# Kernel optimization log

Measured on AMD Instinct MI355X. Metric: run time of the kernel, lower is better.

Reference implementation:

```python
import jax, jax.numpy as jnp
import numpy as np

B, D, C, P = 1024, 768, 150, 64  # batch, in_feats, num_labels, proj2 dim
POS_M, NEG_M = 0.7, 1.4


def setup_inputs() -> dict:
    key = jax.random.key(0)
    ks = jax.random.split(key, 8)
    return {
        "x": jax.random.normal(ks[0], (B, D), jnp.float32),
        "lb": jax.random.randint(ks[1], (B,), 0, C + 1),
        "mem": jax.random.normal(ks[2], (C, D), jnp.float32),
        "fc_w": jax.random.normal(ks[3], (2 * D, 2 * D), jnp.float32) * 0.02,
        "fc_b": jnp.zeros((2 * D,), jnp.float32),
        "p1_w": jax.random.normal(ks[4], (1, 2 * D), jnp.float32) * 0.02,
        "p1_b": jnp.zeros((1,), jnp.float32),
        "p2_w": jax.random.normal(ks[5], (P, 2 * D), jnp.float32) * 0.02,
        "p2_b": jnp.zeros((P,), jnp.float32),
    }


def reference(x, lb, mem, fc_w, fc_b, p1_w, p1_b, p2_w, p2_b):
    d = x.shape[1]
    # cat([a, b], 1) @ fc_w.T == a @ Wx.T + b @ Wm.T  (exact split of the linear)
    Wx, Wm = fc_w[:, :d], fc_w[:, d:]
    xh = x @ Wx.T + fc_b                                # [B, 2D]

    # --- get_logit ---
    seen_h = jax.nn.relu(xh[:, None, :] + mem @ Wm.T)   # [B, C, 2D]
    seen = jnp.einsum('bce,e->bc', seen_h, p1_w[0]) + p1_b[0]   # [B, C]
    uh = jax.nn.relu(xh)                                # cat([x, zeros]) path
    unseen = uh @ p1_w.T + p1_b                         # [B, 1]
    logits = jnp.concatenate([seen, unseen], axis=1)    # [B, C+1]

    # --- masked log-softmax losses (pos_adapte) ---
    labels = jax.nn.one_hot(lb, C + 1, dtype=jnp.float32)
    th = jnp.zeros_like(labels).at[:, -1].set(1.0)
    labels = labels.at[:, -1].set(0.0)
    p_mask = labels + th
    n_mask = 1.0 - labels
    BIG = 1e30
    loss1 = -(jax.nn.log_softmax(logits - (1.0 - p_mask) * BIG, -1) * labels).sum(1)
    loss2 = -(jax.nn.log_softmax(logits - (1.0 - n_mask) * BIG, -1) * th).sum(1)
    loss_cls = (loss1 + loss2).mean()

    # --- metric loss on unseen embedding ---
    u = uh @ p2_w.T + p2_b                              # [B, 64]
    u = u / jnp.maximum(jnp.linalg.norm(u, axis=1, keepdims=True), 1e-12)
    sq_n = (u * u).sum(1)
    sq = sq_n[:, None] + sq_n[None, :] - 2.0 * (u @ u.T)
    err = sq <= 0.0
    dist = jnp.sqrt(jnp.clip(sq, 1e-16, None)) * (~err).astype(u.dtype)
    same = lb[:, None] == lb[None, :]
    eye = jnp.eye(dist.shape[0], dtype=bool)
    pos = (same & ~eye).astype(dist.dtype)
    neg = (~same).astype(dist.dtype)
    pos_l = (jax.nn.relu(dist - POS_M) * pos).sum() / jnp.maximum(pos.sum(), 1.0)
    neg_l = (jax.nn.relu(NEG_M - dist) * neg).sum() / jnp.maximum(neg.sum(), 1.0)

    return loss_cls + pos_l + neg_l
```

## Files before the change

### kernel.cpp

```cpp
#include <hip/hip_runtime.h>
#include <math.h>

#define B_    1024
#define D_    768
#define C_    150
#define P_    64
#define TWOD  1536
#define NCLS  151
#define CPAD  256

#define ECHUNKS 16
#define ECHUNK  96

#define ASTR  40
#define USTRU 120
#define USTR  72

#define NBLK  512

#define OFF_MH      0
#define OFF_XH      (OFF_MH + (C_ * TWOD) / 2)
#define OFF_PARTIAL (OFF_XH + (B_ * TWOD) / 2)
#define OFF_UHF     (OFF_PARTIAL + ECHUNKS * B_ * CPAD)
#define OFF_SQN     (OFF_UHF + (B_ * P_) / 2)
#define OFF_CLS     (OFF_SQN + B_)
#define OFF_PAIR    (OFF_CLS + B_)
#define OFF_BAR     (OFF_PAIR + 1024)

typedef __bf16    bfx8   __attribute__((ext_vector_type(8)));
typedef _Float16  fp16x8 __attribute__((ext_vector_type(8)));
typedef _Float16  h2v    __attribute__((ext_vector_type(2)));
typedef float     f32x4  __attribute__((ext_vector_type(4)));

__device__ inline ushort f2bf(float f) {
    union { float f; unsigned u; } c; c.f = f;
    unsigned r = c.u + 0x7fffu + ((c.u >> 16) & 1u);
    return (ushort)(r >> 16);
}
__device__ inline ushort f2h(float f) {
    _Float16 h = (_Float16)f;
    return __builtin_bit_cast(ushort, h);
}
__device__ inline uint4 pack_bf8(float4 a, float4 b) {
    uint4 r;
    r.x = (unsigned)f2bf(a.x) | ((unsigned)f2bf(a.y) << 16);
    r.y = (unsigned)f2bf(a.z) | ((unsigned)f2bf(a.w) << 16);
    r.z = (unsigned)f2bf(b.x) | ((unsigned)f2bf(b.y) << 16);
    r.w = (unsigned)f2bf(b.z) | ((unsigned)f2bf(b.w) << 16);
    return r;
}
__device__ inline uint4 pack_h8(float4 a, float4 b) {
    uint4 r;
    r.x = (unsigned)f2h(a.x) | ((unsigned)f2h(a.y) << 16);
    r.y = (unsigned)f2h(a.z) | ((unsigned)f2h(a.w) << 16);
    r.z = (unsigned)f2h(b.x) | ((unsigned)f2h(b.y) << 16);
    r.w = (unsigned)f2h(b.z) | ((unsigned)f2h(b.w) << 16);
    return r;
}
__device__ inline unsigned addrelu2(unsigned a, unsigned m) {
    h2v s = __builtin_bit_cast(h2v, a) + __builtin_bit_cast(h2v, m);
    h2v z = {(_Float16)0.f, (_Float16)0.f};
    s = __builtin_elementwise_max(s, z);
    return __builtin_bit_cast(unsigned, s);
}
__device__ inline unsigned relu2(unsigned a) {
    h2v s = __builtin_bit_cast(h2v, a);
    h2v z = {(_Float16)0.f, (_Float16)0.f};
    s = __builtin_elementwise_max(s, z);
    return __builtin_bit_cast(unsigned, s);
}
__device__ inline float dot2acc(unsigned a, unsigned b, float c) {
    return __builtin_amdgcn_fdot2(__builtin_bit_cast(h2v, a),
                                  __builtin_bit_cast(h2v, b), c, false);
}

__device__ __forceinline__ void st_wt_u16(ushort* p, unsigned v) {
    asm volatile("global_store_short %0, %1, off sc0 sc1 nt"
                 :: "v"(p), "v"(v) : "memory");
}
__device__ __forceinline__ void st_wt_f32(float* p, float v) {
    asm volatile("global_store_dword %0, %1, off sc0 sc1 nt"
                 :: "v"(p), "v"(v) : "memory");
}
__device__ __forceinline__ void st_wt_f32x4(float* p, f32x4 v) {
    asm volatile("global_store_dwordx4 %0, %1, off sc0 sc1 nt"
                 :: "v"(p), "v"(v) : "memory");
}

__device__ __forceinline__ void grid_barrier(int* bar, int b)
{
    asm volatile("s_waitcnt vmcnt(0)" ::: "memory");
    __syncthreads();
    if (threadIdx.x == 0) {
        int* arr = bar + (b - 1) * 8 * 16;
        int* gen = bar + 576;
        __hip_atomic_fetch_add(&arr[(blockIdx.x & 7) * 16], 1,
                               __ATOMIC_RELAXED, __HIP_MEMORY_SCOPE_AGENT);
        if (blockIdx.x == 0) {
            for (;;) {
                int s = 0;
#pragma unroll
                for (int k = 0; k < 8; ++k)
                    s += __hip_atomic_load(&arr[k * 16], __ATOMIC_RELAXED,
                                           __HIP_MEMORY_SCOPE_AGENT);
                if (s == NBLK) break;
                __builtin_amdgcn_s_sleep(1);
            }
#pragma unroll
            for (int r = 0; r < 32; ++r)
                __hip_atomic_store(&gen[r * 16], b, __ATOMIC_RELAXED,
                                   __HIP_MEMORY_SCOPE_AGENT);
        } else {
            int* myg = &gen[(blockIdx.x & 31) * 16];
            while (__hip_atomic_load(myg, __ATOMIC_RELAXED,
                                     __HIP_MEMORY_SCOPE_AGENT) < b)
                __builtin_amdgcn_s_sleep(4);
        }
        asm volatile("" ::: "memory");
    }
    __syncthreads();
}

__device__ __forceinline__ void phase_gemm(
    int id, char* smemc,
    const float* __restrict__ x, const float* __restrict__ mem,
    const float* __restrict__ fc_w, const float* __restrict__ fc_b,
    ushort* __restrict__ xh, ushort* __restrict__ mh)
{
    if (id >= 228) return;
    ushort* As = (ushort*)smemc;
    ushort* Bs = (ushort*)(smemc + 64 * ASTR * 2);
    const int t = threadIdx.x;

    const float* A; ushort* Out; int M, m0, n0, koff; bool xblk;
    if (id < 192) {
        xblk = true;  A = x;    Out = xh; M = B_;
        m0 = (id & 15) * 64; n0 = (id >> 4) * 128; koff = 0;
    } else {
        int q = id - 192;
        xblk = false; A = mem;  Out = mh; M = C_;
        m0 = (q % 3) * 64; n0 = (q / 3) * 128; koff = D_;
    }

    const int wave = t >> 6, lane = t & 63;
    const int wm = (wave & 1) * 32, wn = (wave >> 1) * 64;
    const int fm = lane & 15, quad = lane >> 4;

    const int row_a = t >> 2, qa = (t & 3) * 8;
    const int ar = min(m0 + row_a, M - 1);
    const float* Arow = A + (size_t)ar * D_ + qa;
    const float* Brow = fc_w + (size_t)(n0 + row_a) * TWOD + koff + qa;

    f32x4 acc[2][4];
#pragma unroll
    for (int j = 0; j < 4; ++j) {
        float bv = xblk ? fc_b[n0 + wn + j * 16 + fm] : 0.f;
#pragma unroll
        for (int i = 0; i < 2; ++i)
            acc[i][j] = (f32x4){bv, bv, bv, bv};
    }

    float4 pa0  = *(const float4*)(Arow);
    float4 pa1  = *(const float4*)(Arow + 4);
    float4 pb00 = *(const float4*)(Brow);
    float4 pb01 = *(const float4*)(Brow + 4);
    float4 pb10 = *(const float4*)(Brow + 64 * TWOD);
    float4 pb11 = *(const float4*)(Brow + 64 * TWOD + 4);

    for (int k0 = 0; k0 < D_; k0 += 32) {
        __syncthreads();
        *(uint4*)&As[row_a * ASTR + qa]        = pack_bf8(pa0, pa1);
        *(uint4*)&Bs[row_a * ASTR + qa]        = pack_bf8(pb00, pb01);
        *(uint4*)&Bs[(64 + row_a) * ASTR + qa] = pack_bf8(pb10, pb11);
        __syncthreads();
        if (k0 + 32 < D_) {
            pa0  = *(const float4*)(Arow + k0 + 32);
            pa1  = *(const float4*)(Arow + k0 + 36);
            pb00 = *(const float4*)(Brow + k0 + 32);
            pb01 = *(const float4*)(Brow + k0 + 36);
            pb10 = *(const float4*)(Brow + 64 * TWOD + k0 + 32);
            pb11 = *(const float4*)(Brow + 64 * TWOD + k0 + 36);
        }
        bfx8 af[2], bff[4];
#pragma unroll
        for (int i = 0; i < 2; ++i)
            af[i] = *(const bfx8*)&As[(wm + i * 16 + fm) * ASTR + quad * 8];
#pragma unroll
        for (int j = 0; j < 4; ++j)
            bff[j] = *(const bfx8*)&Bs[(wn + j * 16 + fm) * ASTR + quad * 8];
#pragma unroll
        for (int i = 0; i < 2; ++i)
#pragma unroll
            for (int j = 0; j < 4; ++j)
                acc[i][j] = __builtin_amdgcn_mfma_f32_16x16x32_bf16(
                    af[i], bff[j], acc[i][j], 0, 0, 0);
    }

#pragma unroll
    for (int i = 0; i < 2; ++i)
#pragma unroll
        for (int j = 0; j < 4; ++j)
#pragma unroll
            for (int r = 0; r < 4; ++r) {
                int row = m0 + wm + i * 16 + quad * 4 + r;
                int col = n0 + wn + j * 16 + fm;
                if (row < M)
                    st_wt_u16(&Out[(size_t)row * TWOD + col],
                              (unsigned)f2h(acc[i][j][r]));
            }
}

__device__ __forceinline__ void phase_fused(
    int id, char* smem,
    const ushort* __restrict__ xh, const ushort* __restrict__ mh,
    const float* __restrict__ p1w, const float* __restrict__ p2w,
    float* __restrict__ partial)
{
    const int t  = threadIdx.x;
    const int b0 = (id & 7) * 128;
    const int y  = (id >> 3) & 3;
    const int z  = id >> 5;
    const int e0 = z * ECHUNK;

    if (y == 3) {
        ushort* Au = (ushort*)smem;
        ushort* Wu = (ushort*)(smem + 30720);
        const int wave = t >> 6, lane = t & 63;
        const int fm = lane & 15, quad = lane >> 4;

        {
            const int row = t >> 1, kh = (t & 1) * 48;
            const ushort* src = xh + (size_t)(b0 + row) * TWOD + e0 + kh;
            uint4 v[6];
#pragma unroll
            for (int i = 0; i < 6; ++i) v[i] = *(const uint4*)&src[i * 8];
#pragma unroll
            for (int i = 0; i < 6; ++i) {
                v[i].x = relu2(v[i].x); v[i].y = relu2(v[i].y);
                v[i].z = relu2(v[i].z); v[i].w = relu2(v[i].w);
                *(uint4*)&Au[row * USTRU + kh + i * 8] = v[i];
            }
        }
        {
            const int row = t >> 2, ks = (t & 3) * 24;
            const float* pw = p2w + (size_t)row * TWOD + e0 + ks;
#pragma unroll
            for (int i = 0; i < 3; ++i) {
                float4 lo = *(const float4*)&pw[i * 8];
                float4 hi = *(const float4*)&pw[i * 8 + 4];
                *(uint4*)&Wu[row * USTRU + ks + i * 8] = pack_h8(lo, hi);
            }
        }
        __syncthreads();

        f32x4 uacc[2][4];
#pragma unroll
        for (int i = 0; i < 2; ++i)
#pragma unroll
            for (int j = 0; j < 4; ++j) uacc[i][j] = (f32x4){0.f, 0.f, 0.f, 0.f};
#pragma unroll
        for (int k0 = 0; k0 < ECHUNK; k0 += 32) {
            fp16x8 af[2], bff[4];
#pragma unroll
            for (int i = 0; i < 2; ++i)
                af[i] = *(const fp16x8*)&Au[(wave * 32 + i * 16 + fm) * USTRU + k0 + quad * 8];
#pragma unroll
            for (int j = 0; j < 4; ++j)
                bff[j] = *(const fp16x8*)&Wu[(j * 16 + fm) * USTRU + k0 + quad * 8];
#pragma unroll
            for (int i = 0; i < 2; ++i)
#pragma unroll
                for (int j = 0; j < 4; ++j)
                    uacc[i][j] = __builtin_amdgcn_mfma_f32_16x16x32_f16(
                        af[i], bff[j], uacc[i][j], 0, 0, 0);
        }
#pragma unroll
        for (int i = 0; i < 2; ++i)
#pragma unroll
            for (int j = 0; j < 4; ++j)
#pragma unroll
                for (int r = 0; r < 4; ++r) {
                    int row = b0 + wave * 32 + i * 16 + quad * 4 + r;
                    st_wt_f32(&partial[((size_t)z * B_ + row) * CPAD + 192 + j * 16 + fm],
                              uacc[i][j][r]);
                }
        return;
    }

    unsigned* xT = (unsigned*)smem;
    unsigned* mT = (unsigned*)(smem + 24576);
    unsigned* wT = (unsigned*)(smem + 36864);
    const int c0 = y * 64;
    const int tm = t & 15, tn = t >> 4;

    {
        const int row = t >> 1, ph = (t & 1) * 48;
        const ushort* src = xh + (size_t)(b0 + row) * TWOD + e0 + ph;
        uint4 v[6];
#pragma unroll
        for (int i = 0; i < 6; ++i) v[i] = *(const uint4*)&src[i * 8];
#pragma unroll
        for (int i = 0; i < 6; ++i) {
            const int ep = (t & 1) * 24 + i * 4;
            xT[(ep + 0) * 128 + row] = v[i].x;
            xT[(ep + 1) * 128 + row] = v[i].y;
            xT[(ep + 2) * 128 + row] = v[i].z;
            xT[(ep + 3) * 128 + row] = v[i].w;
        }
    }
    {
        const int col = t & 63, seg = t >> 6;
        const int gc  = c0 + col;
        uint4 v[3];
        if (gc < C_) {
            const ushort* src = mh + (size_t)gc * TWOD + e0 + seg * 24;
#pragma unroll
            for (int i = 0; i < 3; ++i) v[i] = *(const uint4*)&src[i * 8];
        } else {
#pragma unroll
            for (int i = 0; i < 3; ++i) v[i] = make_uint4(0, 0, 0, 0);
        }
#pragma unroll
        for (int i = 0; i < 3; ++i) {
            const int ep = seg * 12 + i * 4;
            mT[(ep + 0) * 64 + col] = v[i].x;
            mT[(ep + 1) * 64 + col] = v[i].y;
            mT[(ep + 2) * 64 + col] = v[i].z;
            mT[(ep + 3) * 64 + col] = v[i].w;
        }
    }
    if (t < 12) {
        float4 lo = *(const float4*)&p1w[e0 + t * 8];
        float4 hi = *(const float4*)&p1w[e0 + t * 8 + 4];
        uint4 v = pack_h8(lo, hi);
        wT[t * 4 + 0] = v.x; wT[t * 4 + 1] = v.y;
        wT[t * 4 + 2] = v.z; wT[t * 4 + 3] = v.w;
    }
    __syncthreads();

    float acc[8][4] = {};
#pragma unroll 4
    for (int ep = 0; ep < 48; ++ep) {
        uint4 a0 = *(const uint4*)&xT[ep * 128 + tm * 8];
        uint4 a1 = *(const uint4*)&xT[ep * 128 + tm * 8 + 4];
        uint4 mj = *(const uint4*)&mT[ep * 64 + tn * 4];
        const unsigned wv = wT[ep];
        const unsigned aa[8] = {a0.x, a0.y, a0.z, a0.w, a1.x, a1.y, a1.z, a1.w};
        const unsigned mm[4] = {mj.x, mj.y, mj.z, mj.w};
#pragma unroll
        for (int i = 0; i < 8; ++i)
#pragma unroll
            for (int j = 0; j < 4; ++j)
                acc[i][j] = dot2acc(addrelu2(aa[i], mm[j]), wv, acc[i][j]);
    }

#pragma unroll
    for (int i = 0; i < 8; ++i) {
        const int gb = b0 + tm * 8 + i;
        f32x4 v = {acc[i][0], acc[i][1], acc[i][2], acc[i][3]};
        st_wt_f32x4(&partial[((size_t)z * B_ + gb) * CPAD + c0 + tn * 4], v);
    }
}

__device__ __forceinline__ void phase_reduce(
    char* smemc,
    const float* __restrict__ partial,
    const float* __restrict__ p1b, const float* __restrict__ p2b,
    const int* __restrict__ lb,
    ushort* __restrict__ uhf, float* __restrict__ sqn,
    float* __restrict__ clsbuf)
{
    float* sval = (float*)smemc;
    const int t = threadIdx.x;
    for (int b = blockIdx.x; b < B_; b += NBLK) {
        float v = 0.f;
#pragma unroll
        for (int z = 0; z < ECHUNKS; ++z)
            v += partial[((size_t)z * B_ + b) * CPAD + t];
        if (t < NCLS)       v += p1b[0];
        else if (t >= 192)  v += p2b[t - 192];

        sval[t] = v;
        __syncthreads();

        if (t < 64) {
            float uv = sval[192 + t];
            float s = uv * uv;
#pragma unroll
            for (int off = 32; off; off >>= 1) s += __shfl_xor(s, off);
            float inv = 1.f / fmaxf(sqrtf(s), 1e-12f);
            st_wt_u16(&uhf[(size_t)b * P_ + t], (unsigned)f2h(uv * inv));
            if (t == 0) st_wt_f32(&sqn[b], s * inv * inv);

            const int l = lb[b];
            float mx = -1e30f;
            for (int j = t; j < NCLS; j += 64)
                if (!(j == l && l < C_)) mx = fmaxf(mx, sval[j]);
#pragma unroll
            for (int off = 32; off; off >>= 1) mx = fmaxf(mx, __shfl_xor(mx, off));
            float se = 0.f;
            for (int j = t; j < NCLS; j += 64)
                if (!(j == l && l < C_)) se += expf(sval[j] - mx);
#pragma unroll
            for (int off = 32; off; off >>= 1) se += __shfl_xor(se, off);

            if (t == 0) {
                float l150  = sval[C_];
                float loss2 = mx + logf(se) - l150;
                float loss1 = 0.f;
                if (l < C_) {
                    float a  = sval[l];
                    float m2 = fmaxf(a, l150);
                    loss1 = m2 - a + logf(expf(a - m2) + expf(l150 - m2));
                }
                st_wt_f32(&clsbuf[b], loss1 + loss2);
            }
        }
        __syncthreads();
    }
}

__device__ __forceinline__ void phase_pair(
    int id, char* smemc,
    const ushort* __restrict__ uhf, const float* __restrict__ sqn,
    const int* __restrict__ lb, float* __restrict__ pairpart)
{
    ushort* ui_s = (ushort*)smemc;
    ushort* uj_s = (ushort*)(smemc + 9216);
    float*  sni  = (float*)(smemc + 18432);
    float*  snj  = (float*)(smemc + 18688);
    int*    li   = (int*)(smemc + 18944);
    int*    lj   = (int*)(smemc + 19200);
    float*  red  = (float*)(smemc + 19456);

    const int t  = threadIdx.x;
    const int i0 = (id & 15) * 64, j0 = (id >> 4) * 64;

    for (int idx = t; idx < 512; idx += 256) {
        int row = idx >> 3, ch = (idx & 7) * 8;
        *(uint4*)&ui_s[row * USTR + ch] =
            *(const uint4*)&uhf[(size_t)(i0 + row) * P_ + ch];
        *(uint4*)&uj_s[row * USTR + ch] =
            *(const uint4*)&uhf[(size_t)(j0 + row) * P_ + ch];
    }
    if (t < 64)       { sni[t] = sqn[i0 + t]; li[t] = lb[i0 + t]; }
    else if (t < 128) { int q = t - 64; snj[q] = sqn[j0 + q]; lj[q] = lb[j0 + q]; }
    __syncthreads();

    const int wave = t >> 6, lane = t & 63;
    const int n = lane & 15, quad = lane >> 4;
    const int iw = wave * 16;

    const fp16x8 af0 = *(const fp16x8*)&ui_s[(iw + n) * USTR + quad * 8];
    const fp16x8 af1 = *(const fp16x8*)&ui_s[(iw + n) * USTR + quad * 8 + 32];

    f32x4 acc[4];
#pragma unroll
    for (int jt = 0; jt < 4; ++jt) {
        const fp16x8 bf0 = *(const fp16x8*)&uj_s[(jt * 16 + n) * USTR + quad * 8];
        const fp16x8 bf1 = *(const fp16x8*)&uj_s[(jt * 16 + n) * USTR + quad * 8 + 32];
        acc[jt] = __builtin_amdgcn_mfma_f32_16x16x32_f16(
            af0, bf0, (f32x4){0.f, 0.f, 0.f, 0.f}, 0, 0, 0);
        acc[jt] = __builtin_amdgcn_mfma_f32_16x16x32_f16(
            af1, bf1, acc[jt], 0, 0, 0);
    }

    float ps = 0.f, pc = 0.f, ns = 0.f, nc = 0.f;
#pragma unroll
    for (int jt = 0; jt < 4; ++jt)
#pragma unroll
        for (int r = 0; r < 4; ++r) {
            const int il = iw + quad * 4 + r;
            const int jl = jt * 16 + n;
            float sq = sni[il] + snj[jl] - 2.f * acc[jt][r];
            float dist = sq > 0.f ? sqrtf(fmaxf(sq, 1e-16f)) : 0.f;
            bool same = (li[il] == lj[jl]);
            if (same) {
                if (i0 + il != j0 + jl) { ps += fmaxf(dist - 0.7f, 0.f); pc += 1.f; }
            } else {
                ns += fmaxf(1.4f - dist, 0.f); nc += 1.f;
            }
        }

#pragma unroll
    for (int off = 32; off; off >>= 1) {
        ps += __shfl_xor(ps, off); pc += __shfl_xor(pc, off);
        ns += __shfl_xor(ns, off); nc += __shfl_xor(nc, off);
    }
    if (lane == 0) { red[0 * 4 + wave] = ps; red[1 * 4 + wave] = pc;
                     red[2 * 4 + wave] = ns; red[3 * 4 + wave] = nc; }
    __syncthreads();
    if (t == 0) {
        f32x4 v;
        v[0] = red[0] + red[1] + red[2] + red[3];
        v[1] = red[4] + red[5] + red[6] + red[7];
        v[2] = red[8] + red[9] + red[10] + red[11];
        v[3] = red[12] + red[13] + red[14] + red[15];
        st_wt_f32x4(&pairpart[(size_t)id * 4], v);
    }
}

__device__ __forceinline__ void phase_final(
    char* smemc,
    const float* __restrict__ clsbuf, const float* __restrict__ pairpart,
    float* __restrict__ out)
{
    float* red = (float*)smemc;
    const int t = threadIdx.x;
    float c = clsbuf[t] + clsbuf[t + 256] + clsbuf[t + 512] + clsbuf[t + 768];
    float4 pp = *(const float4*)&pairpart[(size_t)t * 4];
    float ps = pp.x, pc = pp.y, ns = pp.z, nc = pp.w;
#pragma unroll
    for (int off = 32; off; off >>= 1) {
        c  += __shfl_xor(c, off);
        ps += __shfl_xor(ps, off); pc += __shfl_xor(pc, off);
        ns += __shfl_xor(ns, off); nc += __shfl_xor(nc, off);
    }
    const int wave = t >> 6, lane = t & 63;
    if (lane == 0) { red[0 * 4 + wave] = c; red[1 * 4 + wave] = ps;
                     red[2 * 4 + wave] = pc; red[3 * 4 + wave] = ns;
                     red[4 * 4 + wave] = nc; }
    __syncthreads();
    if (t == 0) {
        float C = 0.f, PS = 0.f, PC = 0.f, NS = 0.f, NC = 0.f;
#pragma unroll
        for (int w = 0; w < 4; ++w) {
            C += red[0 * 4 + w]; PS += red[1 * 4 + w]; PC += red[2 * 4 + w];
            NS += red[3 * 4 + w]; NC += red[4 * 4 + w];
        }
        out[0] = C / (float)B_ + PS / fmaxf(PC, 1.f) + NS / fmaxf(NC, 1.f);
    }
}

__global__ __launch_bounds__(256, 2) void mega(
    const float* __restrict__ x, const int* __restrict__ lb,
    const float* __restrict__ mem, const float* __restrict__ fc_w,
    const float* __restrict__ fc_b, const float* __restrict__ p1w,
    const float* __restrict__ p1b, const float* __restrict__ p2w,
    const float* __restrict__ p2b,
    float* ws, float* out)
{
    __shared__ __align__(16) char smem[46080];

    ushort* mh       = (ushort*)(ws + OFF_MH);
    ushort* xh       = (ushort*)(ws + OFF_XH);
    float*  partial  = ws + OFF_PARTIAL;
    ushort* uhf      = (ushort*)(ws + OFF_UHF);
    float*  sqn      = ws + OFF_SQN;
    float*  clsbuf   = ws + OFF_CLS;
    float*  pairpart = ws + OFF_PAIR;
    int*    bar      = (int*)(ws + OFF_BAR);

    const int id = blockIdx.x;

    phase_gemm(id, smem, x, mem, fc_w, fc_b, xh, mh);
    grid_barrier(bar, 1);
    phase_fused(id, smem, xh, mh, p1w, p2w, partial);
    grid_barrier(bar, 2);
    phase_reduce(smem, partial, p1b, p2b, lb, uhf, sqn, clsbuf);
    grid_barrier(bar, 3);
    if (id < 256) phase_pair(id, smem, uhf, sqn, lb, pairpart);

    asm volatile("s_waitcnt vmcnt(0)" ::: "memory");
    __syncthreads();
    if (threadIdx.x == 0) {
        int* arr = bar + 3 * 8 * 16;
        __hip_atomic_fetch_add(&arr[(blockIdx.x & 7) * 16], 1,
                               __ATOMIC_RELAXED, __HIP_MEMORY_SCOPE_AGENT);
    }
    if (blockIdx.x == 0) {
        if (threadIdx.x == 0) {
            int* arr = bar + 3 * 8 * 16;
            for (;;) {
                int s = 0;
#pragma unroll
                for (int k = 0; k < 8; ++k)
                    s += __hip_atomic_load(&arr[k * 16], __ATOMIC_RELAXED,
                                           __HIP_MEMORY_SCOPE_AGENT);
                if (s == NBLK) break;
                __builtin_amdgcn_s_sleep(1);
            }
        }
        asm volatile("" ::: "memory");
        __syncthreads();
        phase_final(smem, clsbuf, pairpart, out);
    }
}

extern "C" void kernel_launch(void* const* d_in, const int* in_sizes, int n_in,
                              void* d_out, int out_size, void* d_ws, size_t ws_size,
                              hipStream_t stream)
{
    const float* x    = (const float*)d_in[0];
    const int*   lb   = (const int*)d_in[1];
    const float* mem  = (const float*)d_in[2];
    const float* fc_w = (const float*)d_in[3];
    const float* fc_b = (const float*)d_in[4];
    const float* p1w  = (const float*)d_in[5];
    const float* p1b  = (const float*)d_in[6];
    const float* p2w  = (const float*)d_in[7];
    const float* p2b  = (const float*)d_in[8];

    float* ws  = (float*)d_ws;
    int*   bar = (int*)(ws + OFF_BAR);

    hipMemsetAsync(bar, 0, 8192, stream);

    mega<<<NBLK, 256, 0, stream>>>(x, lb, mem, fc_w, fc_b,
                                   p1w, p1b, p2w, p2b, ws, (float*)d_out);
}
```

Measured before the change: 140.4 us.

## Shrink GEMM tiles to 64x64, double-buffer LDS with K=64, drop nt store hint

The projection GEMM phase now uses 64x64 output tiles instead of 64x128, doubling the number of work items from 228 to 456 so more of the 512 persistent blocks take part. Each k-step loads 64 columns into double-buffered LDS, which removes one __syncthreads per iteration and halves the number of iterations. The non-temporal hint is also removed from the write-through store helpers. In exchange, each tile reuses its A and B data less, so global traffic for the fc weights rises, and LDS use per block grows.

```diff
diff --git a/kernel.cpp b/kernel.cpp
--- a/kernel.cpp
+++ b/kernel.cpp
@@ -12,7 +12,9 @@
 #define ECHUNKS 16
 #define ECHUNK  96
 
-#define ASTR  40
+#define GSTR  72
+#define GBUF  (64 * GSTR)
+#define NKT   (D_ / 64)
 #define USTRU 120
 #define USTR  72
 
@@ -75,15 +77,15 @@
 }
 
 __device__ __forceinline__ void st_wt_u16(ushort* p, unsigned v) {
-    asm volatile("global_store_short %0, %1, off sc0 sc1 nt"
+    asm volatile("global_store_short %0, %1, off sc0 sc1"
                  :: "v"(p), "v"(v) : "memory");
 }
 __device__ __forceinline__ void st_wt_f32(float* p, float v) {
-    asm volatile("global_store_dword %0, %1, off sc0 sc1 nt"
+    asm volatile("global_store_dword %0, %1, off sc0 sc1"
                  :: "v"(p), "v"(v) : "memory");
 }
 __device__ __forceinline__ void st_wt_f32x4(float* p, f32x4 v) {
-    asm volatile("global_store_dwordx4 %0, %1, off sc0 sc1 nt"
+    asm volatile("global_store_dwordx4 %0, %1, off sc0 sc1"
                  :: "v"(p), "v"(v) : "memory");
 }
 
@@ -127,87 +129,88 @@
     const float* __restrict__ fc_w, const float* __restrict__ fc_b,
     ushort* __restrict__ xh, ushort* __restrict__ mh)
 {
-    if (id >= 228) return;
+    if (id >= 456) return;
     ushort* As = (ushort*)smemc;
-    ushort* Bs = (ushort*)(smemc + 64 * ASTR * 2);
+    ushort* Bs = (ushort*)(smemc + 2 * GBUF * 2);
     const int t = threadIdx.x;
 
     const float* A; ushort* Out; int M, m0, n0, koff; bool xblk;
-    if (id < 192) {
+    if (id < 384) {
         xblk = true;  A = x;    Out = xh; M = B_;
-        m0 = (id & 15) * 64; n0 = (id >> 4) * 128; koff = 0;
+        m0 = (id & 15) * 64; n0 = (id >> 4) * 64; koff = 0;
     } else {
-        int q = id - 192;
+        int q = id - 384;
         xblk = false; A = mem;  Out = mh; M = C_;
-        m0 = (q % 3) * 64; n0 = (q / 3) * 128; koff = D_;
+        m0 = (q % 3) * 64; n0 = (q / 3) * 64; koff = D_;
     }
 
     const int wave = t >> 6, lane = t & 63;
-    const int wm = (wave & 1) * 32, wn = (wave >> 1) * 64;
+    const int wm = wave * 16;
     const int fm = lane & 15, quad = lane >> 4;
 
-    const int row_a = t >> 2, qa = (t & 3) * 8;
+    const int row_a = t >> 2, qa = (t & 3) * 16;
     const int ar = min(m0 + row_a, M - 1);
     const float* Arow = A + (size_t)ar * D_ + qa;
     const float* Brow = fc_w + (size_t)(n0 + row_a) * TWOD + koff + qa;
-
-    f32x4 acc[2][4];
+    const int lw = row_a * GSTR + qa;
+
+    f32x4 acc[4];
 #pragma unroll
     for (int j = 0; j < 4; ++j) {
-        float bv = xblk ? fc_b[n0 + wn + j * 16 + fm] : 0.f;
-#pragma unroll
-        for (int i = 0; i < 2; ++i)
-            acc[i][j] = (f32x4){bv, bv, bv, bv};
-    }
-
-    float4 pa0  = *(const float4*)(Arow);
-    float4 pa1  = *(const float4*)(Arow + 4);
-    float4 pb00 = *(const float4*)(Brow);
-    float4 pb01 = *(const float4*)(Brow + 4);
-    float4 pb10 = *(const float4*)(Brow + 64 * TWOD);
-    float4 pb11 = *(const float4*)(Brow + 64 * TWOD + 4);
-
-    for (int k0 = 0; k0 < D_; k0 += 32) {
+        float bv = xblk ? fc_b[n0 + j * 16 + fm] : 0.f;
+        acc[j] = (f32x4){bv, bv, bv, bv};
+    }
+
+    float4 pa0 = *(const float4*)(Arow);
+    float4 pa1 = *(const float4*)(Arow + 4);
+    float4 pa2 = *(const float4*)(Arow + 8);
+    float4 pa3 = *(const float4*)(Arow + 12);
+    float4 pb0 = *(const float4*)(Brow);
+    float4 pb1 = *(const float4*)(Brow + 4);
+    float4 pb2 = *(const float4*)(Brow + 8);
+    float4 pb3 = *(const float4*)(Brow + 12);
+
+    for (int kt = 0; kt < NKT; ++kt) {
+        ushort* Ad = As + (kt & 1) * GBUF;
+        ushort* Bd = Bs + (kt & 1) * GBUF;
+        *(uint4*)&Ad[lw]     = pack_bf8(pa0, pa1);
+        *(uint4*)&Ad[lw + 8] = pack_bf8(pa2, pa3);
+        *(uint4*)&Bd[lw]     = pack_bf8(pb0, pb1);
+        *(uint4*)&Bd[lw + 8] = pack_bf8(pb2, pb3);
         __syncthreads();
-        *(uint4*)&As[row_a * ASTR + qa]        = pack_bf8(pa0, pa1);
-        *(uint4*)&Bs[row_a * ASTR + qa]        = pack_bf8(pb00, pb01);
-        *(uint4*)&Bs[(64 + row_a) * ASTR + qa] = pack_bf8(pb10, pb11);
-        __syncthreads();
-        if (k0 + 32 < D_) {
-            pa0  = *(const float4*)(Arow + k0 + 32);
-            pa1  = *(const float4*)(Arow + k0 + 36);
-            pb00 = *(const float4*)(Brow + k0 + 32);
-            pb01 = *(const float4*)(Brow + k0 + 36);
-            pb10 = *(const float4*)(Brow + 64 * TWOD + k0 + 32);
-            pb11 = *(const float4*)(Brow + 64 * TWOD + k0 + 36);
-        }
-        bfx8 af[2], bff[4];
-#pragma unroll
-        for (int i = 0; i < 2; ++i)
-            af[i] = *(const bfx8*)&As[(wm + i * 16 + fm) * ASTR + quad * 8];
-#pragma unroll
-        for (int j = 0; j < 4; ++j)
-            bff[j] = *(const bfx8*)&Bs[(wn + j * 16 + fm) * ASTR + quad * 8];
-#pragma unroll
-        for (int i = 0; i < 2; ++i)
-#pragma unroll
-            for (int j = 0; j < 4; ++j)
-                acc[i][j] = __builtin_amdgcn_mfma_f32_16x16x32_bf16(
-                    af[i], bff[j], acc[i][j], 0, 0, 0);
-    }
-
-#pragma unroll
-    for (int i = 0; i < 2; ++i)
-#pragma unroll
-        for (int j = 0; j < 4; ++j)
-#pragma unroll
-            for (int r = 0; r < 4; ++r) {
-                int row = m0 + wm + i * 16 + quad * 4 + r;
-                int col = n0 + wn + j * 16 + fm;
-                if (row < M)
-                    st_wt_u16(&Out[(size_t)row * TWOD + col],
-                              (unsigned)f2h(acc[i][j][r]));
+        if (kt + 1 < NKT) {
+            const int k1 = (kt + 1) * 64;
+            pa0 = *(const float4*)(Arow + k1);
+            pa1 = *(const float4*)(Arow + k1 + 4);
+            pa2 = *(const float4*)(Arow + k1 + 8);
+            pa3 = *(const float4*)(Arow + k1 + 12);
+            pb0 = *(const float4*)(Brow + k1);
+            pb1 = *(const float4*)(Brow + k1 + 4);
+            pb2 = *(const float4*)(Brow + k1 + 8);
+            pb3 = *(const float4*)(Brow + k1 + 12);
+        }
+#pragma unroll
+        for (int ks = 0; ks < 2; ++ks) {
+            bfx8 af = *(const bfx8*)&Ad[(wm + fm) * GSTR + ks * 32 + quad * 8];
+#pragma unroll
+            for (int j = 0; j < 4; ++j) {
+                bfx8 bf = *(const bfx8*)&Bd[(j * 16 + fm) * GSTR + ks * 32 + quad * 8];
+                acc[j] = __builtin_amdgcn_mfma_f32_16x16x32_bf16(
+                    af, bf, acc[j], 0, 0, 0);
             }
+        }
+    }
+
+#pragma unroll
+    for (int j = 0; j < 4; ++j)
+#pragma unroll
+        for (int r = 0; r < 4; ++r) {
+            int row = m0 + wm + quad * 4 + r;
+            int col = n0 + j * 16 + fm;
+            if (row < M)
+                st_wt_u16(&Out[(size_t)row * TWOD + col],
+                          (unsigned)f2h(acc[j][r]));
+        }
 }
 
 __device__ __forceinline__ void phase_fused(
```

New measurement: 132.7 us. -5.5%, faster.
